# Performance work log

Measured on AMD Instinct MI355X. Metric: run time of the kernel, lower is better.

The kernel has to match this reference:

```python
import jax, jax.numpy as jnp
import numpy as np

HD, CD, BN = 128, 192, 16       # hidden_dim, context_dim, bin_num
OC = 2 * HD                     # ProjectionInputDepth out_chs
GC = HD + OC + CD               # GRU conv in-channels = hidden + (out_chs + context)
MAX_TREE_DEPTH = 6


def conv2d(x, w, b, ph, pw):
    y = jax.lax.conv_general_dilated(
        x, w, window_strides=(1, 1), padding=((ph, ph), (pw, pw)),
        dimension_numbers=('NCHW', 'OIHW', 'NCHW'))
    return y + b[None, :, None, None]


def setup_inputs():
    key = jax.random.key(0)
    B, H, W = 2, 120, 160
    ki = iter(jax.random.split(key, 20))
    def w(shape, s=0.05):
        return jax.random.normal(next(ki), shape, jnp.float32) * s
    z = lambda c: jnp.zeros((c,), jnp.float32)
    return {
        'depth': jax.random.uniform(next(ki), (B, 1, H, W), jnp.float32) * 80.0,
        'context': jax.random.normal(next(ki), (B, CD, H, W), jnp.float32),
        'gru_hidden': jax.random.normal(next(ki), (B, HD, H, W), jnp.float32),
        'encd1_w': w((HD, BN, 7, 7)), 'encd1_b': z(HD),
        'encd2_w': w((HD, HD, 3, 3)), 'encd2_b': z(HD),
        'encd3_w': w((HD, HD, 3, 3)), 'encd3_b': z(HD),
        'encd4_w': w((OC, HD, 3, 3)), 'encd4_b': z(OC),
        'convz1_w': w((HD, GC, 1, 5)), 'convz1_b': z(HD),
        'convr1_w': w((HD, GC, 1, 5)), 'convr1_b': z(HD),
        'convq1_w': w((HD, GC, 1, 5)), 'convq1_b': z(HD),
        'convz2_w': w((HD, GC, 5, 1)), 'convz2_b': z(HD),
        'convr2_w': w((HD, GC, 5, 1)), 'convr2_b': z(HD),
        'convq2_w': w((HD, GC, 5, 1)), 'convq2_b': z(HD),
        'ph1_w': w((HD, HD, 3, 3)), 'ph1_b': z(HD),
        'ph2_w': w((BN, HD, 3, 3)), 'ph2_b': z(BN),
        'bin_num': 16, 'min_depth': 0, 'max_depth': 80,
    }


def reference(depth, context, gru_hidden,
              encd1_w, encd1_b, encd2_w, encd2_b, encd3_w, encd3_b, encd4_w, encd4_b,
              convz1_w, convz1_b, convr1_w, convr1_b, convq1_w, convq1_b,
              convz2_w, convz2_b, convr2_w, convr2_b, convq2_w, convq2_b,
              ph1_w, ph1_b, ph2_w, ph2_b,
              bin_num, min_depth, max_depth):
    sg = jax.lax.stop_gradient
    B, _, H, W = depth.shape
    n = int(bin_num)
    mn, mx = float(min_depth), float(max_depth)
    # get_iebins: uniform bin edges via cumsum of constant intervals, (B, n+1, H, W)
    iv0 = jnp.concatenate([jnp.full((B, 1, H, W), mn, jnp.float32),
                           jnp.full((B, n, H, W), (mx - mn) / n, jnp.float32)], axis=1)
    bin_edges = jnp.cumsum(iv0, axis=1)
    current_depths = 0.5 * (bin_edges[:, :-1] + bin_edges[:, 1:])
    h = gru_hidden
    rs, cs, us = [], [], []
    for _ in range(MAX_TREE_DEPTH):
        cd = sg(current_depths)
        # ProjectionInputDepth
        d = jax.nn.relu(conv2d(cd, encd1_w, encd1_b, 3, 3))
        d = jax.nn.relu(conv2d(d, encd2_w, encd2_b, 1, 1))
        d = jax.nn.relu(conv2d(d, encd3_w, encd3_b, 1, 1))
        d = jax.nn.relu(conv2d(d, encd4_w, encd4_b, 1, 1))
        x = jnp.concatenate([d, context], axis=1)
        # SepConvGRU: horizontal (1,5) pass then vertical (5,1) pass
        hx = jnp.concatenate([h, x], axis=1)
        zg = jax.nn.sigmoid(conv2d(hx, convz1_w, convz1_b, 0, 2))
        rg = jax.nn.sigmoid(conv2d(hx, convr1_w, convr1_b, 0, 2))
        q = jnp.tanh(conv2d(jnp.concatenate([rg * h, x], axis=1), convq1_w, convq1_b, 0, 2))
        h = (1.0 - zg) * h + zg * q
        hx = jnp.concatenate([h, x], axis=1)
        zg = jax.nn.sigmoid(conv2d(hx, convz2_w, convz2_b, 2, 0))
        rg = jax.nn.sigmoid(conv2d(hx, convr2_w, convr2_b, 2, 0))
        q = jnp.tanh(conv2d(jnp.concatenate([rg * h, x], axis=1), convq2_w, convq2_b, 2, 0))
        h = (1.0 - zg) * h + zg * q
        # PHead -> per-bin probabilities
        prob = jax.nn.softmax(conv2d(jax.nn.relu(conv2d(h, ph1_w, ph1_b, 1, 1)), ph2_w, ph2_b, 1, 1), axis=1)
        depth_r = jnp.sum(prob * cd, axis=1, keepdims=True)        # (B,1,H,W)
        rs.append(depth_r)
        unc = jnp.sqrt(jnp.sum(prob * (cd - depth_r) ** 2, axis=1, keepdims=True))
        us.append(unc)
        # get_label: bin i with edges[i] <= d < edges[i+1]; 0 if out of range
        dv = sg(depth_r[:, 0])                                     # (B,H,W)
        cnt = jnp.sum((dv[:, None] >= bin_edges[:, 1:n]).astype(jnp.int32), axis=1)
        label = jnp.where(dv >= bin_edges[:, n], 0, cnt)[:, None]  # (B,1,H,W)
        cs.append(jnp.take_along_axis(cd, label, axis=1))
        # update_bins (mode 'direct', no grad): recenter on depth_r, width = uncertainty
        dr, um = sg(depth_r), sg(unc)
        start = jnp.maximum(dr - 0.5 * um, mn)
        ivals = jnp.concatenate([start, jnp.broadcast_to(um / n, (B, n, H, W))], axis=1)
        bin_edges = jnp.clip(jnp.cumsum(ivals, axis=1), mn, mx)
        current_depths = 0.5 * (bin_edges[:, :-1] + bin_edges[:, 1:])
    # stacked lists: (3, 6, B, 1, H, W) = [pred_depths_r, pred_depths_c, uncertainty_maps]
    return jnp.stack([jnp.stack(rs), jnp.stack(cs), jnp.stack(us)])
```

## Files before the change

kernel.cpp:

```cpp
#include <hip/hip_runtime.h>
#include <hip/hip_bf16.h>


#define HD  128
#define CDC 192
#define BN  16
#define OCH 256
#define GC  576
#define NB  2
#define HH  120
#define WW  160
#define HW  (HH*WW)
#define BHW (NB*HW)
#define PXT (BHW/128)
#define GXP (((PXT+7)/8)*8)
#define TPX (GXP/8)
#define PWW 168
#define PHH 126
#define PHW (PWW*PHH)
#define POFF(y,x) (((y)+3)*PWW + (x) + 4)

__device__ __forceinline__ float2 ldf2(const float* p){ return *(const float2*)p; }
__device__ __forceinline__ void stf2(float* p, float a, float b){
  *(float2*)p = make_float2(a,b);
}

typedef float f2 __attribute__((ext_vector_type(2), aligned(4)));
__device__ __forceinline__ f2 ldpo(const float* __restrict__ base, const unsigned off){
  return *(const f2*)(base + off);
}
__device__ __forceinline__ f2 ldw2(const float* __restrict__ p){ return *(const f2*)p; }

__device__ __forceinline__ void pkfma2(f2& a, const f2 v, const f2 w){
  a = __builtin_elementwise_fma(v, w, a);
}

__global__ __launch_bounds__(256) void k_zero32(float* __restrict__ p, const size_t n){
  const size_t i = (size_t)blockIdx.x*256 + threadIdx.x;
  for (size_t k=i; k<n; k += (size_t)gridDim.x*256) p[k] = 0.f;
}
__global__ __launch_bounds__(256) void k_zero64(double* __restrict__ p, const size_t n){
  const size_t i = (size_t)blockIdx.x*256 + threadIdx.x;
  for (size_t k=i; k<n; k += (size_t)gridDim.x*256) p[k] = 0.0;
}

__global__ __launch_bounds__(256) void k_pad(const float* __restrict__ src,
        float* __restrict__ dst, const int nplanes){
  const int i = blockIdx.x*256 + threadIdx.x;
  if (i >= nplanes*HW) return;
  const int bc = i / HW, r = i - bc*HW;
  const int y = r / WW, x = r - y*WW;
  dst[(size_t)bc*PHW + POFF(y,x)] = src[i];
}

__global__ __launch_bounds__(256) void k_init(const float* __restrict__ gh,
        float* __restrict__ h, double* __restrict__ edges, double* __restrict__ cdp){
  const int i = blockIdx.x*256 + threadIdx.x;
  const int nh = NB*HD*HW;
  if (i < nh){
    const int bc = i / HW, r = i - bc*HW;
    const int y = r / WW, x = r - y*WW;
    h[(size_t)bc*PHW + POFF(y,x)] = gh[i];
  }
  if (i < BHW){
    const int b = i / HW, r = i - b*HW;
    const int y = r / WW, x = r - y*WW;
    const int pr = POFF(y,x);
    double e = 0.0;
    #pragma unroll
    for (int k=0;k<BN;++k){
      edges[(b*(BN+1)+k)*HW + r] = e;
      cdp[((size_t)b*BN+k)*PHW + pr] = e + 2.5;
      e += 5.0;
    }
    edges[(b*(BN+1)+BN)*HW + r] = e;
  }
}

__global__ __launch_bounds__(256) void k_wxpose(const float* __restrict__ w,
        float* __restrict__ wt, const int Cout, const int CIN, const int TAPS,
        const int n){
  const int i = blockIdx.x*256 + threadIdx.x;
  if (i >= n) return;
  const int ct = CIN*TAPS;
  const int o = i / ct;
  const int rem = i - o*ct;
  const int c = rem / TAPS;
  const int t = rem - c*TAPS;
  wt[((size_t)c*TAPS + t)*Cout + o] = w[i];
}

template<int GY>
__device__ __forceinline__ bool blk_decode(int& xs, int& yg){
  const int id  = blockIdx.x;
  const int xcd = id & 7;
  const int s   = id >> 3;
  yg = s & (GY-1);
  const int k = s / GY;
  xs = xcd*TPX + k;
  return xs < PXT;
}

__device__ __forceinline__ void pair_decode(const int xs, int& b, int& r0, int& po){
  const int lane = threadIdx.x & 63;
  const int pb = xs*128;
  b = pb / HW;
  r0 = pb - b*HW + 2*lane;
  const int y = r0 / WW, x = r0 - y*WW;
  po = POFF(y,x);
}

__global__ __launch_bounds__(256) void k_e1(const double* __restrict__ cdp,
        const float* __restrict__ wt, const float* __restrict__ bias,
        float* __restrict__ out){
  const int NACC = 8, NP = NACC/2;
  int xs, yg;
  if (!blk_decode<4>(xs, yg)) return;
  const int wvu = __builtin_amdgcn_readfirstlane((int)(threadIdx.x >> 6));
  const int ow0 = (yg*4 + wvu)*NACC;
  int b, r0, po;
  pair_decode(xs, b, r0, po);
  double acc[2][NACC];
  #pragma unroll
  for (int j=0;j<NACC;++j){
    const double bj = (double)bias[ow0+j];
    acc[0][j]=bj; acc[1][j]=bj;
  }
  const double* inb = cdp + (size_t)b*16*PHW;
  #pragma unroll 1
  for (int t=0;t<49;++t){
    const unsigned pot = (unsigned)(po + (t/7 - 3)*PWW + (t%7 - 3));
    f2 ca[2][NP];
    #pragma unroll
    for (int p=0;p<NP;++p){ ca[0][p]=f2{0.f,0.f}; ca[1][p]=f2{0.f,0.f}; }
    const float* wr = wt + (size_t)t*HD + ow0;
    #pragma unroll 4
    for (int c=0;c<16;++c){
      const double* pp = inb + (size_t)c*PHW;
      const float v0 = (float)pp[pot];
      const float v1 = (float)pp[pot+1u];
      const f2 v00 = {v0, v0};
      const f2 v11 = {v1, v1};
      #pragma unroll
      for (int p=0;p<NP;++p){
        const f2 wp_ = ldw2(wr + 2*p);
        pkfma2(ca[0][p], v00, wp_);
        pkfma2(ca[1][p], v11, wp_);
      }
      wr += (size_t)49*HD;
    }
    #pragma unroll
    for (int p=0;p<NP;++p){
      acc[0][2*p]  +=(double)ca[0][p].x; acc[0][2*p+1]+=(double)ca[0][p].y;
      acc[1][2*p]  +=(double)ca[1][p].x; acc[1][2*p+1]+=(double)ca[1][p].y;
    }
  }
  #pragma unroll
  for (int j=0;j<NACC;++j){
    double v0 = acc[0][j]; v0 = v0>0.0?v0:0.0;
    double v1 = acc[1][j]; v1 = v1>0.0?v1:0.0;
    stf2(out + ((size_t)b*HD + ow0 + j)*PHW + po, (float)v0, (float)v1);
  }
}

template<int NACC,int GY,int ACT>
__global__ __launch_bounds__(256) void k_fc3(const float* __restrict__ in,
        const float* __restrict__ wt, const float* __restrict__ bias,
        float* __restrict__ out, const int Cout){
  const int NP = NACC/2;
  int xs, yg;
  if (!blk_decode<GY>(xs, yg)) return;
  const int wvu = __builtin_amdgcn_readfirstlane((int)(threadIdx.x >> 6));
  const int ow0 = (yg*4 + wvu)*NACC;
  int b, r0, po;
  pair_decode(xs, b, r0, po);
  double acc[2][NACC];
  #pragma unroll
  for (int j=0;j<NACC;++j){
    const double bj = (double)bias[ow0+j];
    acc[0][j]=bj; acc[1][j]=bj;
  }
  const float* inb = in + (size_t)b*128*PHW;
  #pragma unroll 1
  for (int t=0;t<9;++t){
    const unsigned pot = (unsigned)(po + (t/3 - 1)*PWW + (t%3 - 1));
    #pragma unroll 1
    for (int c0=0;c0<128;c0+=32){
      f2 ca[2][NP];
      #pragma unroll
      for (int p=0;p<NP;++p){ ca[0][p]=f2{0.f,0.f}; ca[1][p]=f2{0.f,0.f}; }
      const float* wr = wt + ((size_t)c0*9 + t)*Cout + ow0;
      #pragma unroll 8
      for (int c=0;c<32;++c){
        const f2 v = ldpo(inb + (size_t)(c0+c)*PHW, pot);
        const f2 v00 = {v.x, v.x};
        const f2 v11 = {v.y, v.y};
        #pragma unroll
        for (int p=0;p<NP;++p){
          const f2 wp_ = ldw2(wr + 2*p);
          pkfma2(ca[0][p], v00, wp_);
          pkfma2(ca[1][p], v11, wp_);
        }
        wr += (size_t)9*Cout;
      }
      #pragma unroll
      for (int p=0;p<NP;++p){
        acc[0][2*p]  +=(double)ca[0][p].x; acc[0][2*p+1]+=(double)ca[0][p].y;
        acc[1][2*p]  +=(double)ca[1][p].x; acc[1][2*p+1]+=(double)ca[1][p].y;
      }
    }
  }
  #pragma unroll
  for (int j=0;j<NACC;++j){
    double v0 = acc[0][j], v1 = acc[1][j];
    if (ACT==1){ v0 = v0>0.0?v0:0.0; v1 = v1>0.0?v1:0.0; }
    stf2(out + ((size_t)b*Cout + ow0 + j)*PHW + po, (float)v0, (float)v1);
  }
}

template<int C,int NACC>
__device__ __forceinline__ void seg2(const float* __restrict__ plane, const unsigned pot,
    const float* __restrict__ wz0, const float* __restrict__ wr0,
    double az[2][NACC], double ar[2][NACC]){
  const int NP = NACC/2;
  #pragma unroll 1
  for (int c0=0;c0<C;c0+=32){
    f2 cz[2][NP], cr[2][NP];
    #pragma unroll
    for (int p=0;p<NP;++p){
      cz[0][p]=f2{0.f,0.f}; cz[1][p]=f2{0.f,0.f};
      cr[0][p]=f2{0.f,0.f}; cr[1][p]=f2{0.f,0.f};
    }
    const float* wz = wz0 + (size_t)c0*5*HD;
    const float* wr = wr0 + (size_t)c0*5*HD;
    #pragma unroll 4
    for (int c=0;c<32;++c){
      const f2 v = ldpo(plane + (size_t)(c0+c)*PHW, pot);
      const f2 v00 = {v.x, v.x};
      const f2 v11 = {v.y, v.y};
      #pragma unroll
      for (int p=0;p<NP;++p){
        const f2 wzp = ldw2(wz + 2*p);
        const f2 wrp = ldw2(wr + 2*p);
        pkfma2(cz[0][p], v00, wzp); pkfma2(cz[1][p], v11, wzp);
        pkfma2(cr[0][p], v00, wrp); pkfma2(cr[1][p], v11, wrp);
      }
      wz += 5*HD; wr += 5*HD;
    }
    #pragma unroll
    for (int p=0;p<NP;++p){
      az[0][2*p]+=(double)cz[0][p].x; az[0][2*p+1]+=(double)cz[0][p].y;
      az[1][2*p]+=(double)cz[1][p].x; az[1][2*p+1]+=(double)cz[1][p].y;
      ar[0][2*p]+=(double)cr[0][p].x; ar[0][2*p+1]+=(double)cr[0][p].y;
      ar[1][2*p]+=(double)cr[1][p].x; ar[1][2*p+1]+=(double)cr[1][p].y;
    }
  }
}
template<int C,int NACC>
__device__ __forceinline__ void seg3(const float* __restrict__ plane, const unsigned pot,
    const float* __restrict__ wz0, const float* __restrict__ wr0,
    const float* __restrict__ wq0,
    double az[2][NACC], double ar[2][NACC], double aq[2][NACC]){
  const int NP = NACC/2;
  #pragma unroll 1
  for (int c0=0;c0<C;c0+=32){
    f2 cz[2][NP], cr[2][NP], cq[2][NP];
    #pragma unroll
    for (int p=0;p<NP;++p){
      cz[0][p]=f2{0.f,0.f}; cz[1][p]=f2{0.f,0.f};
      cr[0][p]=f2{0.f,0.f}; cr[1][p]=f2{0.f,0.f};
      cq[0][p]=f2{0.f,0.f}; cq[1][p]=f2{0.f,0.f};
    }
    const float* wz = wz0 + (size_t)c0*5*HD;
    const float* wr = wr0 + (size_t)c0*5*HD;
    const float* wq = wq0 + (size_t)c0*5*HD;
    #pragma unroll 4
    for (int c=0;c<32;++c){
      const f2 v = ldpo(plane + (size_t)(c0+c)*PHW, pot);
      const f2 v00 = {v.x, v.x};
      const f2 v11 = {v.y, v.y};
      #pragma unroll
      for (int p=0;p<NP;++p){
        const f2 wzp = ldw2(wz + 2*p);
        const f2 wrp = ldw2(wr + 2*p);
        const f2 wqp = ldw2(wq + 2*p);
        pkfma2(cz[0][p], v00, wzp); pkfma2(cz[1][p], v11, wzp);
        pkfma2(cr[0][p], v00, wrp); pkfma2(cr[1][p], v11, wrp);
        pkfma2(cq[0][p], v00, wqp); pkfma2(cq[1][p], v11, wqp);
      }
      wz += 5*HD; wr += 5*HD; wq += 5*HD;
    }
    #pragma unroll
    for (int p=0;p<NP;++p){
      az[0][2*p]+=(double)cz[0][p].x; az[0][2*p+1]+=(double)cz[0][p].y;
      az[1][2*p]+=(double)cz[1][p].x; az[1][2*p+1]+=(double)cz[1][p].y;
      ar[0][2*p]+=(double)cr[0][p].x; ar[0][2*p+1]+=(double)cr[0][p].y;
      ar[1][2*p]+=(double)cr[1][p].x; ar[1][2*p+1]+=(double)cr[1][p].y;
      aq[0][2*p]+=(double)cq[0][p].x; aq[0][2*p+1]+=(double)cq[0][p].y;
      aq[1][2*p]+=(double)cq[1][p].x; aq[1][2*p+1]+=(double)cq[1][p].y;
    }
  }
}
template<int C,int NACC>
__device__ __forceinline__ void seg1(const float* __restrict__ plane, const unsigned pot,
    const float* __restrict__ wq0, double aq[2][NACC]){
  const int NP = NACC/2;
  #pragma unroll 1
  for (int c0=0;c0<C;c0+=32){
    f2 cq[2][NP];
    #pragma unroll
    for (int p=0;p<NP;++p){ cq[0][p]=f2{0.f,0.f}; cq[1][p]=f2{0.f,0.f}; }
    const float* wq = wq0 + (size_t)c0*5*HD;
    #pragma unroll 8
    for (int c=0;c<32;++c){
      const f2 v = ldpo(plane + (size_t)(c0+c)*PHW, pot);
      const f2 v00 = {v.x, v.x};
      const f2 v11 = {v.y, v.y};
      #pragma unroll
      for (int p=0;p<NP;++p){
        const f2 wqp = ldw2(wq + 2*p);
        pkfma2(cq[0][p], v00, wqp);
        pkfma2(cq[1][p], v11, wqp);
      }
      wq += 5*HD;
    }
    #pragma unroll
    for (int p=0;p<NP;++p){
      aq[0][2*p]+=(double)cq[0][p].x; aq[0][2*p+1]+=(double)cq[0][p].y;
      aq[1][2*p]+=(double)cq[1][p].x; aq[1][2*p+1]+=(double)cq[1][p].y;
    }
  }
}

template<int VERT>
__global__ __launch_bounds__(256) void k_zrx(
    const float* __restrict__ h, const float* __restrict__ d4,
    const float* __restrict__ ctxp,
    const float* __restrict__ wtz, const float* __restrict__ wtr,
    const float* __restrict__ wtq,
    const float* __restrict__ bz, const float* __restrict__ br,
    const float* __restrict__ bq,
    float* __restrict__ zg, float* __restrict__ rgh, float* __restrict__ qx){
  const int NACC = 4;
  int xs, yg;
  if (!blk_decode<8>(xs, yg)) return;
  const int wvu = __builtin_amdgcn_readfirstlane((int)(threadIdx.x >> 6));
  const int ow0 = (yg*4 + wvu)*NACC;
  int b, r0, po;
  pair_decode(xs, b, r0, po);
  double az[2][NACC], ar[2][NACC], aq[2][NACC];
  #pragma unroll
  for (int j=0;j<NACC;++j){
    const double bzj=(double)bz[ow0+j], brj=(double)br[ow0+j], bqj=(double)bq[ow0+j];
    az[0][j]=bzj; az[1][j]=bzj; ar[0][j]=brj; ar[1][j]=brj; aq[0][j]=bqj; aq[1][j]=bqj;
  }
  const float* hb = h   + (size_t)b*HD *PHW;
  const float* db = d4  + (size_t)b*OCH*PHW;
  const float* cb = ctxp+ (size_t)b*CDC*PHW;
  #pragma unroll 1
  for (int t=0;t<5;++t){
    const unsigned pot = (unsigned)(po + (VERT ? (t-2)*PWW : (t-2)));
    seg2<HD ,NACC>(hb, pot, wtz + (size_t)t*HD + ow0,
                            wtr + (size_t)t*HD + ow0, az, ar);
    seg3<OCH,NACC>(db, pot, wtz + ((size_t)HD*5 + t)*HD + ow0,
                            wtr + ((size_t)HD*5 + t)*HD + ow0,
                            wtq + ((size_t)HD*5 + t)*HD + ow0, az, ar, aq);
    seg3<CDC,NACC>(cb, pot, wtz + ((size_t)(HD+OCH)*5 + t)*HD + ow0,
                            wtr + ((size_t)(HD+OCH)*5 + t)*HD + ow0,
                            wtq + ((size_t)(HD+OCH)*5 + t)*HD + ow0, az, ar, aq);
  }
  #pragma unroll
  for (int j=0;j<NACC;++j){
    const size_t pp = ((size_t)b*HD + ow0 + j)*PHW + po;
    const float2 hv = ldf2(h + pp);
    const double z0 = 1.0/(1.0+exp(-az[0][j])), z1 = 1.0/(1.0+exp(-az[1][j]));
    const double g0 = (1.0/(1.0+exp(-ar[0][j]))) * (double)hv.x;
    const double g1 = (1.0/(1.0+exp(-ar[1][j]))) * (double)hv.y;
    stf2(zg  + pp, (float)z0, (float)z1);
    stf2(rgh + pp, (float)g0, (float)g1);
    stf2(qx + ((size_t)b*HD + ow0 + j)*HW + r0, (float)aq[0][j], (float)aq[1][j]);
  }
}

template<int VERT>
__global__ __launch_bounds__(256) void k_qh(
    const float* __restrict__ rgh, const float* __restrict__ wtq,
    const float* __restrict__ qx, const float* __restrict__ zg,
    float* __restrict__ h){
  const int NACC = 8;
  int xs, yg;
  if (!blk_decode<4>(xs, yg)) return;
  const int wvu = __builtin_amdgcn_readfirstlane((int)(threadIdx.x >> 6));
  const int ow0 = (yg*4 + wvu)*NACC;
  int b, r0, po;
  pair_decode(xs, b, r0, po);
  double aq[2][NACC];
  #pragma unroll
  for (int j=0;j<NACC;++j){
    const float2 q0 = ldf2(qx + ((size_t)b*HD + ow0 + j)*HW + r0);
    aq[0][j] = (double)q0.x; aq[1][j] = (double)q0.y;
  }
  const float* gb = rgh + (size_t)b*HD*PHW;
  #pragma unroll 1
  for (int t=0;t<5;++t){
    const unsigned pot = (unsigned)(po + (VERT ? (t-2)*PWW : (t-2)));
    seg1<HD,NACC>(gb, pot, wtq + (size_t)t*HD + ow0, aq);
  }
  #pragma unroll
  for (int j=0;j<NACC;++j){
    const size_t pp = ((size_t)b*HD + ow0 + j)*PHW + po;
    const float2 zv = ldf2(zg + pp);
    const float2 hv = ldf2(h  + pp);
    const double z0=(double)zv.x, z1=(double)zv.y;
    const double n0 = (1.0-z0)*(double)hv.x + z0*tanh(aq[0][j]);
    const double n1 = (1.0-z1)*(double)hv.y + z1*tanh(aq[1][j]);
    stf2(h + pp, (float)n0, (float)n1);
  }
}

__global__ __launch_bounds__(256) void k_stats(const float* __restrict__ lg,
    double* __restrict__ edges, double* __restrict__ cdp, float* __restrict__ out,
    const int it){
  const int px = blockIdx.x*256 + threadIdx.x;
  const int b = px / HW, r = px - b*HW;
  const int y = r / WW, x = r - y*WW;
  const int pr = POFF(y,x);
  double l[BN], p[BN], c[BN];
  double m = -1e300;
  #pragma unroll
  for (int k=0;k<BN;++k){ l[k] = (double)lg[((size_t)b*BN+k)*PHW + pr]; m = l[k]>m?l[k]:m; }
  double s = 0.0;
  #pragma unroll
  for (int k=0;k<BN;++k){ p[k] = exp(l[k]-m); s += p[k]; }
  double dr = 0.0;
  #pragma unroll
  for (int k=0;k<BN;++k){ c[k] = cdp[((size_t)b*BN+k)*PHW + pr]; p[k] = p[k]/s; dr += p[k]*c[k]; }
  double var = 0.0;
  #pragma unroll
  for (int k=0;k<BN;++k){ const double d = c[k]-dr; var += p[k]*(d*d); }
  const double un = sqrt(var);
  int cnt = 0;
  #pragma unroll
  for (int k=1;k<BN;++k) cnt += (dr >= edges[(b*(BN+1)+k)*HW + r]) ? 1 : 0;
  const double etop = edges[(b*(BN+1)+BN)*HW + r];
  const int label = (dr >= etop) ? 0 : cnt;
  double csv = c[0];
  #pragma unroll
  for (int k=1;k<BN;++k) csv = (label==k) ? c[k] : csv;
  out[((0*6+it)*NB + b)*HW + r] = (float)dr;
  out[((1*6+it)*NB + b)*HW + r] = (float)csv;
  out[((2*6+it)*NB + b)*HW + r] = (float)un;
  const double start = dr - 0.5*un > 0.0 ? dr - 0.5*un : 0.0;
  const double step = un * (1.0/BN);
  double e = start;
  double prev = e < 0.0 ? 0.0 : (e > 80.0 ? 80.0 : e);
  edges[(b*(BN+1)+0)*HW + r] = prev;
  #pragma unroll
  for (int k=1;k<=BN;++k){
    e = e + step;
    const double ec = e < 0.0 ? 0.0 : (e > 80.0 ? 80.0 : e);
    edges[(b*(BN+1)+k)*HW + r] = ec;
    cdp[((size_t)b*BN + (k-1))*PHW + pr] = 0.5*(prev + ec);
    prev = ec;
  }
}

extern "C" void kernel_launch(void* const* d_in, const int* in_sizes, int n_in,
                              void* d_out, int out_size, void* d_ws, size_t ws_size,
                              hipStream_t stream){
  const float* ctx = (const float*)d_in[1];
  const float* gh  = (const float*)d_in[2];
  const float *e1w=(const float*)d_in[3],  *e1b=(const float*)d_in[4];
  const float *e2w=(const float*)d_in[5],  *e2b=(const float*)d_in[6];
  const float *e3w=(const float*)d_in[7],  *e3b=(const float*)d_in[8];
  const float *e4w=(const float*)d_in[9],  *e4b=(const float*)d_in[10];
  const float *z1w=(const float*)d_in[11], *z1b=(const float*)d_in[12];
  const float *r1w=(const float*)d_in[13], *r1b=(const float*)d_in[14];
  const float *q1w=(const float*)d_in[15], *q1b=(const float*)d_in[16];
  const float *z2w=(const float*)d_in[17], *z2b=(const float*)d_in[18];
  const float *r2w=(const float*)d_in[19], *r2b=(const float*)d_in[20];
  const float *q2w=(const float*)d_in[21], *q2b=(const float*)d_in[22];
  const float *p1w=(const float*)d_in[23], *p1b=(const float*)d_in[24];
  const float *p2w=(const float*)d_in[25], *p2b=(const float*)d_in[26];
  float* out = (float*)d_out;

  double* edges = (double*)d_ws;
  double* cdp   = edges + (size_t)NB*(BN+1)*HW;
  float* fb    = (float*)(cdp + (size_t)NB*BN*PHW);
  float* hp    = fb;
  float* d4p   = hp    + (size_t)NB*HD *PHW;
  float* bufAp = d4p   + (size_t)NB*OCH*PHW;
  float* bufBp = bufAp + (size_t)NB*HD *PHW;
  float* ctxp  = bufBp + (size_t)NB*HD *PHW;
  float* lgtsp = ctxp  + (size_t)NB*CDC*PHW;
  const size_t npad32 = (size_t)NB*(HD+OCH+HD+HD+CDC+BN)*PHW;
  float* qx   = lgtsp + (size_t)NB*BN*PHW;
  float* wp   = qx + (size_t)NB*HD*HW;
  float* we1 = wp;              wp += (size_t)HD*16*49;
  float* we2 = wp;              wp += (size_t)HD*HD*9;
  float* we3 = wp;              wp += (size_t)HD*HD*9;
  float* we4 = wp;              wp += (size_t)OCH*HD*9;
  float* wz1 = wp;              wp += (size_t)HD*GC*5;
  float* wr1 = wp;              wp += (size_t)HD*GC*5;
  float* wq1 = wp;              wp += (size_t)HD*GC*5;
  float* wz2 = wp;              wp += (size_t)HD*GC*5;
  float* wr2 = wp;              wp += (size_t)HD*GC*5;
  float* wq2 = wp;              wp += (size_t)HD*GC*5;
  float* wp1 = wp;              wp += (size_t)HD*HD*9;
  float* wp2 = wp;              wp += (size_t)16*HD*9;

  const dim3 blk(256);

  k_zero32<<<dim3(2048), blk, 0, stream>>>(fb, npad32);
  k_zero64<<<dim3(1024), blk, 0, stream>>>(cdp, (size_t)NB*BN*PHW);

  #define XP(src,dst,Cout_,CIN_,TAPS_) { const int n=(Cout_)*(CIN_)*(TAPS_); \
    k_wxpose<<<dim3((n+255)/256), blk, 0, stream>>>(src, dst, Cout_, CIN_, TAPS_, n); }
  XP(e1w, we1, HD, 16, 49); XP(e2w, we2, HD, HD, 9); XP(e3w, we3, HD, HD, 9);
  XP(e4w, we4, OCH, HD, 9);
  XP(z1w, wz1, HD, GC, 5); XP(r1w, wr1, HD, GC, 5); XP(q1w, wq1, HD, GC, 5);
  XP(z2w, wz2, HD, GC, 5); XP(r2w, wr2, HD, GC, 5); XP(q2w, wq2, HD, GC, 5);
  XP(p1w, wp1, HD, HD, 9); XP(p2w, wp2, 16, HD, 9);
  #undef XP

  k_pad<<<dim3((NB*CDC*HW+255)/256), blk, 0, stream>>>(ctx, ctxp, NB*CDC);
  k_init<<<dim3((NB*HD*HW+255)/256), blk, 0, stream>>>(gh, hp, edges, cdp);

  const int G8 = GXP*8, G4 = GXP*4, G1 = GXP;
  const int PXB = BHW/256;

  for (int it=0; it<6; ++it){
    k_e1        <<<dim3(G4), blk, 0, stream>>>(cdp,   we1, e1b, bufAp);
    k_fc3<8,4,1><<<dim3(G4), blk, 0, stream>>>(bufAp, we2, e2b, bufBp, HD);
    k_fc3<8,4,1><<<dim3(G4), blk, 0, stream>>>(bufBp, we3, e3b, bufAp, HD);
    k_fc3<8,8,1><<<dim3(G8), blk, 0, stream>>>(bufAp, we4, e4b, d4p,  OCH);
    k_zrx<0><<<dim3(G8), blk, 0, stream>>>(hp, d4p, ctxp, wz1, wr1, wq1,
                                           z1b, r1b, q1b, bufAp, bufBp, qx);
    k_qh <0><<<dim3(G4), blk, 0, stream>>>(bufBp, wq1, qx, bufAp, hp);
    k_zrx<1><<<dim3(G8), blk, 0, stream>>>(hp, d4p, ctxp, wz2, wr2, wq2,
                                           z2b, r2b, q2b, bufAp, bufBp, qx);
    k_qh <1><<<dim3(G4), blk, 0, stream>>>(bufBp, wq2, qx, bufAp, hp);
    k_fc3<8,4,1><<<dim3(G4), blk, 0, stream>>>(hp,    wp1, p1b, bufAp, HD);
    k_fc3<4,1,0><<<dim3(G1), blk, 0, stream>>>(bufAp, wp2, p2b, lgtsp, 16);
    k_stats<<<dim3(PXB), blk, 0, stream>>>(lgtsp, edges, cdp, out, it);
  }
}
```

Before: 25.21 ms.

## Rebalance GRU gate kernel work across a fixed persistent-style grid

The z/r/x gate convolution kernel now launches a fixed grid of 2048 blocks, and each wave processes a contiguous range of (pixel-tile, output-channel-pair) work items. Adjacent pairs within the same tile are fused into a 4-accumulator sweep, falling back to 2 accumulators at range edges. The aim is to even out wave load and reduce tail imbalance compared with the previous fixed 8-way channel split. The cost is more loop control and a sweep that is sometimes narrower, which reuses the input loads less.

```diff
diff --git a/kernel.cpp b/kernel.cpp
--- a/kernel.cpp
+++ b/kernel.cpp
@@ -15,6 +15,7 @@
 #define PXT (BHW/128)
 #define GXP (((PXT+7)/8)*8)
 #define TPX (GXP/8)
+#define ZPAIRS (TPX*64)
 #define PWW 168
 #define PHH 126
 #define PHW (PWW*PHH)
@@ -332,8 +333,8 @@
   }
 }
 
-template<int VERT>
-__global__ __launch_bounds__(256) void k_zrx(
+template<int VERT,int NACC>
+__device__ __forceinline__ void zrx_sweep(const int xs, const int ow0,
     const float* __restrict__ h, const float* __restrict__ d4,
     const float* __restrict__ ctxp,
     const float* __restrict__ wtz, const float* __restrict__ wtr,
@@ -341,11 +342,6 @@
     const float* __restrict__ bz, const float* __restrict__ br,
     const float* __restrict__ bq,
     float* __restrict__ zg, float* __restrict__ rgh, float* __restrict__ qx){
-  const int NACC = 4;
-  int xs, yg;
-  if (!blk_decode<8>(xs, yg)) return;
-  const int wvu = __builtin_amdgcn_readfirstlane((int)(threadIdx.x >> 6));
-  const int ow0 = (yg*4 + wvu)*NACC;
   int b, r0, po;
   pair_decode(xs, b, r0, po);
   double az[2][NACC], ar[2][NACC], aq[2][NACC];
@@ -379,6 +375,40 @@
     stf2(zg  + pp, (float)z0, (float)z1);
     stf2(rgh + pp, (float)g0, (float)g1);
     stf2(qx + ((size_t)b*HD + ow0 + j)*HW + r0, (float)aq[0][j], (float)aq[1][j]);
+  }
+}
+
+template<int VERT>
+__global__ __launch_bounds__(256) void k_zrx(
+    const float* __restrict__ h, const float* __restrict__ d4,
+    const float* __restrict__ ctxp,
+    const float* __restrict__ wtz, const float* __restrict__ wtr,
+    const float* __restrict__ wtq,
+    const float* __restrict__ bz, const float* __restrict__ br,
+    const float* __restrict__ bq,
+    float* __restrict__ zg, float* __restrict__ rgh, float* __restrict__ qx){
+  const int wvu = __builtin_amdgcn_readfirstlane((int)(threadIdx.x >> 6));
+  const int xcd   = blockIdx.x & 7;
+  const int bslot = blockIdx.x >> 3;
+  const int w = bslot*4 + wvu;
+  int p         = (w*ZPAIRS) >> 10;
+  const int pend = ((w+1)*ZPAIRS) >> 10;
+  #pragma unroll 1
+  while (p < pend){
+    const int tk = p >> 6;
+    const int xs = xcd*TPX + tk;
+    if (xs >= PXT) break;
+    const int pr = p & 63;
+    const bool fuse = (p+1 < pend) && (((p+1) >> 6) == tk);
+    if (fuse){
+      zrx_sweep<VERT,4>(xs, pr*2, h, d4, ctxp, wtz, wtr, wtq,
+                        bz, br, bq, zg, rgh, qx);
+      p += 2;
+    } else {
+      zrx_sweep<VERT,2>(xs, pr*2, h, d4, ctxp, wtz, wtr, wtq,
+                        bz, br, bq, zg, rgh, qx);
+      p += 1;
+    }
   }
 }
 
@@ -527,6 +557,7 @@
   k_init<<<dim3((NB*HD*HW+255)/256), blk, 0, stream>>>(gh, hp, edges, cdp);
 
   const int G8 = GXP*8, G4 = GXP*4, G1 = GXP;
+  const int GZ = 2048;
   const int PXB = BHW/256;
 
   for (int it=0; it<6; ++it){
@@ -534,10 +565,10 @@
     k_fc3<8,4,1><<<dim3(G4), blk, 0, stream>>>(bufAp, we2, e2b, bufBp, HD);
     k_fc3<8,4,1><<<dim3(G4), blk, 0, stream>>>(bufBp, we3, e3b, bufAp, HD);
     k_fc3<8,8,1><<<dim3(G8), blk, 0, stream>>>(bufAp, we4, e4b, d4p,  OCH);
-    k_zrx<0><<<dim3(G8), blk, 0, stream>>>(hp, d4p, ctxp, wz1, wr1, wq1,
+    k_zrx<0><<<dim3(GZ), blk, 0, stream>>>(hp, d4p, ctxp, wz1, wr1, wq1,
                                            z1b, r1b, q1b, bufAp, bufBp, qx);
     k_qh <0><<<dim3(G4), blk, 0, stream>>>(bufBp, wq1, qx, bufAp, hp);
-    k_zrx<1><<<dim3(G8), blk, 0, stream>>>(hp, d4p, ctxp, wz2, wr2, wq2,
+    k_zrx<1><<<dim3(GZ), blk, 0, stream>>>(hp, d4p, ctxp, wz2, wr2, wq2,
                                            z2b, r2b, q2b, bufAp, bufBp, qx);
     k_qh <1><<<dim3(G4), blk, 0, stream>>>(bufBp, wq2, qx, bufAp, hp);
     k_fc3<8,4,1><<<dim3(G4), blk, 0, stream>>>(hp,    wp1, p1b, bufAp, HD);
```

After: 36.93 ms. 1.46x slower.
